# Kernel optimization log

Measured on AMD Instinct MI355X. Metric: run time of the kernel, lower is better.

The kernel has to match this reference:

```python
import jax, jax.numpy as jnp
import numpy as np

E, H, L = 512, 1024, 2
SRC_V, TGT_V = 32000, 32000
B, S, T = 32, 128, 128
BOS = 1  # vocab.Vocab.bos_idx


def _lstm_layer(x, h0, c0, Wih, Whh, bih, bhh):
    """Single-direction LSTM layer. x: [B, S, D] -> (ys [B,S,H], hT, cT).
    PyTorch gate order: i, f, g, o."""
    b = bih + bhh
    def step(carry, xt):
        h, c = carry
        gates = xt @ Wih.T + h @ Whh.T + b          # [B, 4H]
        i, f, g, o = jnp.split(gates, 4, axis=-1)
        i = jax.nn.sigmoid(i)
        f = jax.nn.sigmoid(f)
        g = jnp.tanh(g)
        o = jax.nn.sigmoid(o)
        c = f * c + i * g
        h = o * jnp.tanh(c)
        return (h, c), h
    (hT, cT), ys = jax.lax.scan(step, (h0, c0), jnp.swapaxes(x, 0, 1))
    return jnp.swapaxes(ys, 0, 1), hT, cT


def _stacked_lstm(x, h0s, c0s, params):
    """params: list of (Wih, Whh, bih, bhh) per layer. h0s/c0s: [L, B, H]."""
    hs, cs = [], []
    y = x
    for l, (Wih, Whh, bih, bhh) in enumerate(params):
        y, hT, cT = _lstm_layer(y, h0s[l], c0s[l], Wih, Whh, bih, bhh)
        hs.append(hT)
        cs.append(cT)
    return y, jnp.stack(hs), jnp.stack(cs)


def setup_inputs() -> dict:
    key = jax.random.key(0)
    ks = jax.random.split(key, 24)
    sc = 1.0 / np.sqrt(H)
    inp = {}
    inp["src"] = jax.random.randint(ks[0], (B, S), 0, SRC_V)
    inp["tgt"] = jax.random.randint(ks[1], (B, T), 0, TGT_V)
    inp["enc_emb"] = jax.random.normal(ks[2], (SRC_V, E), jnp.float32)
    inp["dec_emb"] = jax.random.normal(ks[3], (TGT_V, E), jnp.float32)
    i = 4
    for pre in ("enc", "dec"):
        for l in range(L):
            din = E if l == 0 else H
            inp[f"{pre}_Wih{l}"] = jax.random.uniform(ks[i + 0], (4 * H, din), jnp.float32, -sc, sc)
            inp[f"{pre}_Whh{l}"] = jax.random.uniform(ks[i + 1], (4 * H, H), jnp.float32, -sc, sc)
            inp[f"{pre}_bih{l}"] = jax.random.uniform(ks[i + 2], (4 * H,), jnp.float32, -sc, sc)
            inp[f"{pre}_bhh{l}"] = jax.random.uniform(ks[i + 3], (4 * H,), jnp.float32, -sc, sc)
            i += 4
    return inp


def reference(src, tgt, enc_emb, dec_emb,
              enc_Wih0, enc_Whh0, enc_bih0, enc_bhh0,
              enc_Wih1, enc_Whh1, enc_bih1, enc_bhh1,
              dec_Wih0, dec_Whh0, dec_bih0, dec_bhh0,
              dec_Wih1, dec_Whh1, dec_bih1, dec_bhh1):
    enc_params = [(enc_Wih0, enc_Whh0, enc_bih0, enc_bhh0),
                  (enc_Wih1, enc_Whh1, enc_bih1, enc_bhh1)]
    dec_params = [(dec_Wih0, dec_Whh0, dec_bih0, dec_bhh0),
                  (dec_Wih1, dec_Whh1, dec_bih1, dec_bhh1)]
    # Encoder: full-sequence LSTM from zero state
    x = enc_emb[src]                                  # [B, S, E]
    zeros = jnp.zeros((L, B, H), x.dtype)
    enc_out, h, c = _stacked_lstm(x, zeros, zeros, enc_params)
    # Decoder: teacher-forced inputs = [BOS, tgt[:, :-1]]
    dec_in = jnp.concatenate(
        [jnp.full((B, 1), BOS, tgt.dtype), tgt[:, :-1]], axis=1)  # [B, T]
    y = dec_emb[dec_in]                               # [B, T, E]
    dec_out, _, _ = _stacked_lstm(y, h, c, dec_params)
    return dec_out                                    # [B, T, H]
```

## Files before the change

### kernel.cpp

```cpp
#include <hip/hip_runtime.h>
#include <hip/hip_bf16.h>
#include <stdint.h>


typedef __attribute__((ext_vector_type(8))) __bf16 bf16x8;
typedef __attribute__((ext_vector_type(4))) __bf16 bf16x4;
typedef __attribute__((ext_vector_type(4))) float  f32x4;

#define SLAB 32768
#define RNN_SMEM (65536 + 65536 + 512)

__device__ __forceinline__ float sigmoidf_(float x) {
  return 1.f / (1.f + __expf(-x));
}
__device__ __forceinline__ float tanhf_(float x) {
  float e = __expf(-2.f * fabsf(x));
  float t = (1.f - e) / (1.f + e);
  return x < 0.f ? -t : t;
}

__global__ void init_ws(float* zeros, unsigned* flags) {
  int i = blockIdx.x * 256 + threadIdx.x;
  if (i < 32 * 1024) zeros[i] = 0.f;
  if (i < 512) flags[i] = 0u;
}

__global__ void gather_emb(const int* __restrict__ src, const int* __restrict__ tgt,
                           const float* __restrict__ ee, const float* __restrict__ de,
                           __bf16* __restrict__ Xe, __bf16* __restrict__ Xd) {
  int row = blockIdx.x & 4095;
  int t = row >> 5, b = row & 31;
  bool isd = blockIdx.x >= 4096;
  int tok = isd ? (t == 0 ? 1 : tgt[b * 128 + t - 1]) : src[b * 128 + t];
  const float* ep = (isd ? de : ee) + (size_t)tok * 512;
  __bf16* op = (isd ? Xd : Xe) + (size_t)row * 512;
  int i = threadIdx.x * 4;
  float4 v = *(const float4*)(ep + i);
  bf16x4 t4;
  t4[0] = (__bf16)v.x; t4[1] = (__bf16)v.y; t4[2] = (__bf16)v.z; t4[3] = (__bf16)v.w;
  *(bf16x4*)(op + i) = t4;
}

__global__ __launch_bounds__(256) void gemm_xp(
    const __bf16* __restrict__ A, const float* __restrict__ W,
    const float* __restrict__ bih, const float* __restrict__ bhh,
    __bf16* __restrict__ C, int K) {
  __shared__ char sA[128 * 64 * 2];
  __shared__ char sB[128 * 64 * 2];
  int tid = threadIdx.x;
  int lane = tid & 63, wave = tid >> 6;
  int wm = wave & 1, wn = wave >> 1;
  int bm = blockIdx.x & 31, bn = blockIdx.x >> 5;
  int frow = lane & 15;
  int kj = (lane >> 4) * 16;

  f32x4 acc[4][4] = {};

  for (int k0 = 0; k0 < K; k0 += 64) {
#pragma unroll
    for (int c4 = 0; c4 < 4; ++c4) {
      int idx = (c4 * 256 + tid) * 8;
      int r = idx >> 6, kk = idx & 63;
      bf16x8 v = *(const bf16x8*)(A + (size_t)(bm * 128 + r) * K + k0 + kk);
      *(bf16x8*)(sA + ((r * 128 + kk * 2) ^ ((r & 7) << 4))) = v;
    }
#pragma unroll
    for (int c4 = 0; c4 < 4; ++c4) {
      int idx = (c4 * 256 + tid) * 8;
      int r = idx >> 6, kk = idx & 63;
      const float* wp = W + (size_t)(bn * 128 + r) * K + k0 + kk;
      float4 w0 = *(const float4*)wp;
      float4 w1 = *(const float4*)(wp + 4);
      bf16x8 v;
      v[0] = (__bf16)w0.x; v[1] = (__bf16)w0.y; v[2] = (__bf16)w0.z; v[3] = (__bf16)w0.w;
      v[4] = (__bf16)w1.x; v[5] = (__bf16)w1.y; v[6] = (__bf16)w1.z; v[7] = (__bf16)w1.w;
      *(bf16x8*)(sB + ((r * 128 + kk * 2) ^ ((r & 7) << 4))) = v;
    }
    __syncthreads();
#pragma unroll
    for (int half = 0; half < 2; ++half) {
      int kb = half * 64 + kj;
      bf16x8 af[4], bfr[4];
#pragma unroll
      for (int f = 0; f < 4; ++f) {
        int arr = wm * 64 + f * 16 + frow;
        af[f] = *(const bf16x8*)(sA + (arr * 128 + (kb ^ ((arr & 7) << 4))));
        int brr = wn * 64 + f * 16 + frow;
        bfr[f] = *(const bf16x8*)(sB + (brr * 128 + (kb ^ ((brr & 7) << 4))));
      }
#pragma unroll
      for (int fm = 0; fm < 4; ++fm)
#pragma unroll
        for (int fn = 0; fn < 4; ++fn)
          acc[fm][fn] = __builtin_amdgcn_mfma_f32_16x16x32_bf16(af[fm], bfr[fn],
                                                                acc[fm][fn], 0, 0, 0);
    }
    __syncthreads();
  }
  int cm = bm * 128 + wm * 64, cn = bn * 128 + wn * 64;
#pragma unroll
  for (int fn = 0; fn < 4; ++fn) {
    int col = cn + fn * 16 + frow;
    int g = col >> 10, hcol = col & 1023;
    int blkd = hcol >> 3, hl = hcol & 7;
    float bias = bih[col] + bhh[col];
#pragma unroll
    for (int fm = 0; fm < 4; ++fm) {
      int r0 = cm + fm * 16 + ((lane >> 4) << 2);
#pragma unroll
      for (int j = 0; j < 4; ++j) {
        int row = r0 + j;
        C[(size_t)(row >> 5) * 131072 + blkd * 1024 + hl * 128 + g * 32 +
          (row & 31)] = (__bf16)(acc[fm][fn][j] + bias);
      }
    }
  }
}

struct RnnArgs {
  const float* Whh;
  const float* Wxh;
  const float* bih;
  const float* bhh;
  const __bf16* XP;
  const __bf16* xslab;
  const unsigned* xflags;
  const __bf16* h0;
  const float* c0;
  __bf16* hseq;
  float* cfin;
  float* yout;
  unsigned* flags;
};

__device__ __forceinline__ void wait128(const unsigned* fl, unsigned t) {
  int lane = threadIdx.x & 63;
  for (;;) {
    bool ok = (__hip_atomic_load(fl + lane, __ATOMIC_RELAXED,
                                 __HIP_MEMORY_SCOPE_AGENT) >= t) &&
              (__hip_atomic_load(fl + 64 + lane, __ATOMIC_RELAXED,
                                 __HIP_MEMORY_SCOPE_AGENT) >= t);
    if (__all(ok)) return;
    __builtin_amdgcn_s_sleep(1);
  }
}

__device__ __forceinline__ f32x4 accum_k1024_sw(f32x4 acc, const char* bbase,
                                                const char* aRow, int swz, int kj) {
#pragma unroll
  for (int kt = 0; kt < 32; kt += 8) {
    bf16x8 bv[8];
#pragma unroll
    for (int u = 0; u < 8; ++u)
      bv[u] = *(const bf16x8*)(bbase + (size_t)(kt + u) * 2048);
#pragma unroll
    for (int u = 0; u < 8; ++u) {
      int kb = (kt + u) * 64 + kj;
      bf16x8 av = *(const bf16x8*)(aRow + (kb ^ swz));
      acc = __builtin_amdgcn_mfma_f32_16x16x32_bf16(av, bv[u], acc, 0, 0, 0);
    }
  }
  return acc;
}

__device__ __forceinline__ void rnn_body(const RnnArgs& P, int blk, char* smem) {
  char*   sW0 = smem;
  char*   sW1 = smem + 65536;
  __bf16* sP  = (__bf16*)(smem + 131072);

  int tid = threadIdx.x;
  int lane = tid & 63, wave = tid >> 6;
  int mt = wave & 1, nt = wave >> 1;
  bool isL0 = (P.XP != nullptr);

  __builtin_amdgcn_fence(__ATOMIC_ACQUIRE, "agent");

  {
    const float* srcs[2] = {P.Wxh, P.Whh};
    char* dsts[2] = {sW0, sW1};
    for (int s = (isL0 ? 1 : 0); s < 2; ++s) {
      for (int g = 0; g < 4; ++g) {
        const float* sp = srcs[s] + (size_t)(g * 1024 + blk * 8) * 1024;
#pragma unroll
        for (int it = 0; it < 8; ++it) {
          int e = (it * 256 + tid) * 4;
          int rl = e >> 10, k = e & 1023;
          float4 v = *(const float4*)(sp + e);
          bf16x4 t4;
          t4[0] = (__bf16)v.x; t4[1] = (__bf16)v.y;
          t4[2] = (__bf16)v.z; t4[3] = (__bf16)v.w;
          int r = rl * 4 + g;
          *(bf16x4*)(dsts[s] + ((r << 11) + ((k << 1) ^ ((r & 7) << 4)))) = t4;
        }
      }
    }
  }

  int hl = mt * 4 + (lane >> 4);
  int b  = nt * 16 + (lane & 15);
  float c = P.c0[b * 1024 + blk * 8 + hl];

  float bI = 0.f, bF = 0.f, bG = 0.f, bO = 0.f;
  if (!isL0) {
    int col = blk * 8 + hl;
    bI = P.bih[col] + P.bhh[col];
    bF = P.bih[1024 + col] + P.bhh[1024 + col];
    bG = P.bih[2048 + col] + P.bhh[2048 + col];
    bO = P.bih[3072 + col] + P.bhh[3072 + col];
  }

  int rr  = mt * 16 + (lane & 15);
  int swz = (rr & 7) << 4;
  const char* aRow0 = sW0 + (rr << 11);
  const char* aRow1 = sW1 + (rr << 11);
  int kj   = (lane >> 4) * 16;
  int bsub = (lane >> 4) * 512 + b * 16;

  const __bf16* xpb = isL0 ? (P.XP + (size_t)blk * 1024 + hl * 128 + b) : nullptr;

  for (int t = 0; t < 128; ++t) {
    float xi = bI, xf = bF, xg = bG, xo = bO;
    if (isL0) {
      const __bf16* xr = xpb + (size_t)t * 131072;
      xi = (float)xr[0];  xf = (float)xr[32];
      xg = (float)xr[64]; xo = (float)xr[96];
    }

    const char* hb = (const char*)((t == 0) ? P.h0
                                            : (P.hseq + (size_t)(t - 1) * SLAB)) + bsub;
    f32x4 acc = {0.f, 0.f, 0.f, 0.f};

    if (isL0) {
      if (wave == 0 && t > 0) wait128(P.flags, (unsigned)t);
      __syncthreads();
      acc = accum_k1024_sw(acc, hb, aRow1, swz, kj);
    } else {
      if (wave == 0) wait128(P.xflags, (unsigned)(t + 1));
      __syncthreads();
      const char* xb = (const char*)(P.xslab + (size_t)t * SLAB) + bsub;
      acc = accum_k1024_sw(acc, xb, aRow0, swz, kj);
      if (wave == 0 && t > 0) wait128(P.flags, (unsigned)t);
      __syncthreads();
      acc = accum_k1024_sw(acc, hb, aRow1, swz, kj);
    }

    float gi = sigmoidf_(acc[0] + xi);
    float gf = sigmoidf_(acc[1] + xf);
    float gg = tanhf_(acc[2] + xg);
    float go = sigmoidf_(acc[3] + xo);
    c = gf * c + gi * gg;
    float h = go * tanhf_(c);
    sP[b * 8 + hl] = (__bf16)h;
    __syncthreads();

    if (tid < 64) {
      unsigned long long v = *(const unsigned long long*)(sP + tid * 4);
      unsigned long long* dst = (unsigned long long*)(
          (char*)P.hseq + (size_t)t * 65536 + blk * 512 + tid * 8);
      __hip_atomic_store(dst, v, __ATOMIC_RELAXED, __HIP_MEMORY_SCOPE_AGENT);
      asm volatile("s_waitcnt vmcnt(0)" ::: "memory");
      if (tid == 0)
        __hip_atomic_store(P.flags + blk, (unsigned)(t + 1), __ATOMIC_RELEASE,
                           __HIP_MEMORY_SCOPE_AGENT);
    }
    if (P.yout) {
      int yb = tid >> 3, yhl = tid & 7;
      P.yout[((size_t)yb * 128 + t) * 1024 + blk * 8 + yhl] =
          (float)sP[yb * 8 + yhl];
    }
  }
  P.cfin[b * 1024 + blk * 8 + hl] = c;
}

__global__ __launch_bounds__(256) void rnn_pair(RnnArgs A, RnnArgs B) {
  extern __shared__ char smem[];
  if (blockIdx.x < 128) rnn_body(A, blockIdx.x, smem);
  else                  rnn_body(B, blockIdx.x - 128, smem);
}

extern "C" void kernel_launch(void* const* d_in, const int* in_sizes, int n_in,
                              void* d_out, int out_size, void* d_ws, size_t ws_size,
                              hipStream_t stream) {
  (void)in_sizes; (void)n_in; (void)out_size; (void)ws_size;
  const int*   src     = (const int*)d_in[0];
  const int*   tgt     = (const int*)d_in[1];
  const float* enc_emb = (const float*)d_in[2];
  const float* dec_emb = (const float*)d_in[3];
  const float* W[16];
  for (int i = 0; i < 16; ++i) W[i] = (const float*)d_in[4 + i];

  char* ws = (char*)d_ws;
  size_t off = 0;
  auto alloc = [&](size_t bytes) {
    char* p = ws + off;
    off += (bytes + 255) & ~(size_t)255;
    return p;
  };
  unsigned* flags = (unsigned*)alloc((size_t)4 * 128 * sizeof(unsigned));
  float*    zeros = (float*)alloc((size_t)32 * 1024 * 4);
  __bf16*   Xe   = (__bf16*)alloc((size_t)4096 * 512 * 2);
  __bf16*   Xd   = (__bf16*)alloc((size_t)4096 * 512 * 2);
  __bf16*   XP1  = (__bf16*)alloc((size_t)4096 * 4096 * 2);
  __bf16*   XP2  = (__bf16*)alloc((size_t)4096 * 4096 * 2);
  __bf16*   hE0  = (__bf16*)alloc((size_t)128 * SLAB * 2);
  __bf16*   hE1  = (__bf16*)alloc((size_t)128 * SLAB * 2);
  __bf16*   hD0  = (__bf16*)alloc((size_t)128 * SLAB * 2);
  __bf16*   hD1  = (__bf16*)alloc((size_t)128 * SLAB * 2);
  float*    cE0  = (float*)alloc((size_t)32 * 1024 * 4);
  float*    cE1  = (float*)alloc((size_t)32 * 1024 * 4);
  float*    cd0  = (float*)alloc((size_t)32 * 1024 * 4);
  float*    cd1  = (float*)alloc((size_t)32 * 1024 * 4);

  hipFuncSetAttribute((const void*)rnn_pair,
                      hipFuncAttributeMaxDynamicSharedMemorySize, RNN_SMEM);

  init_ws<<<128, 256, 0, stream>>>(zeros, flags);
  gather_emb<<<8192, 128, 0, stream>>>(src, tgt, enc_emb, dec_emb, Xe, Xd);

  gemm_xp<<<1024, 256, 0, stream>>>(Xe, W[0], W[2], W[3], XP1, 512);
  gemm_xp<<<1024, 256, 0, stream>>>(Xd, W[8], W[10], W[11], XP2, 512);

  unsigned* fE0 = flags;
  unsigned* fE1 = flags + 128;
  unsigned* fD0 = flags + 256;
  unsigned* fD1 = flags + 384;

  RnnArgs e0{W[1], nullptr, nullptr, nullptr, XP1, nullptr, nullptr,
             (const __bf16*)zeros, zeros, hE0, cE0, nullptr, fE0};
  RnnArgs e1{W[5], W[4], W[6], W[7], nullptr, hE0, fE0,
             (const __bf16*)zeros, zeros, hE1, cE1, nullptr, fE1};
  rnn_pair<<<256, 256, RNN_SMEM, stream>>>(e0, e1);

  RnnArgs d0{W[9], nullptr, nullptr, nullptr, XP2, nullptr, nullptr,
             hE0 + (size_t)127 * SLAB, cE0, hD0, cd0, nullptr, fD0};
  RnnArgs d1{W[13], W[12], W[14], W[15], nullptr, hD0, fD0,
             hE1 + (size_t)127 * SLAB, cE1, hD1, cd1, (float*)d_out, fD1};
  rnn_pair<<<256, 256, RNN_SMEM, stream>>>(d0, d1);
}
```

Before: 2.141 ms.

## Prefetch layer-1 input slab into registers one step ahead and merge waits

Splits the recurrent body into separate layer-0 and layer-1 paths. The layer-1 path double-buffers its input-slab fragments in registers, loading step t+1's x data after finishing step t. It also merges the xflags and flags spin-waits into a single poll and drops one barrier per step. Launch bounds are set to one block per SM so the larger register footprint (64 bf16x8 fragments plus h fragments) fits, at the risk of register pressure or spills.

```diff
diff --git a/kernel.cpp b/kernel.cpp
--- a/kernel.cpp
+++ b/kernel.cpp
@@ -216,63 +216,139 @@
   int kj   = (lane >> 4) * 16;
   int bsub = (lane >> 4) * 512 + b * 16;
 
-  const __bf16* xpb = isL0 ? (P.XP + (size_t)blk * 1024 + hl * 128 + b) : nullptr;
-
-  for (int t = 0; t < 128; ++t) {
-    float xi = bI, xf = bF, xg = bG, xo = bO;
-    if (isL0) {
+  if (isL0) {
+    const __bf16* xpb = P.XP + (size_t)blk * 1024 + hl * 128 + b;
+    for (int t = 0; t < 128; ++t) {
       const __bf16* xr = xpb + (size_t)t * 131072;
-      xi = (float)xr[0];  xf = (float)xr[32];
-      xg = (float)xr[64]; xo = (float)xr[96];
-    }
-
-    const char* hb = (const char*)((t == 0) ? P.h0
-                                            : (P.hseq + (size_t)(t - 1) * SLAB)) + bsub;
-    f32x4 acc = {0.f, 0.f, 0.f, 0.f};
-
-    if (isL0) {
+      float pxi = (float)xr[0];  float pxf = (float)xr[32];
+      float pxg = (float)xr[64]; float pxo = (float)xr[96];
+
+      const char* hb = (const char*)((t == 0) ? P.h0
+                         : (P.hseq + (size_t)(t - 1) * SLAB)) + bsub;
+      f32x4 acc = {0.f, 0.f, 0.f, 0.f};
+
       if (wave == 0 && t > 0) wait128(P.flags, (unsigned)t);
       __syncthreads();
       acc = accum_k1024_sw(acc, hb, aRow1, swz, kj);
-    } else {
-      if (wave == 0) wait128(P.xflags, (unsigned)(t + 1));
+
+      float gi = sigmoidf_(acc[0] + pxi);
+      float gf = sigmoidf_(acc[1] + pxf);
+      float gg = tanhf_(acc[2] + pxg);
+      float go = sigmoidf_(acc[3] + pxo);
+      c = gf * c + gi * gg;
+      float h = go * tanhf_(c);
+      sP[b * 8 + hl] = (__bf16)h;
       __syncthreads();
-      const char* xb = (const char*)(P.xslab + (size_t)t * SLAB) + bsub;
-      acc = accum_k1024_sw(acc, xb, aRow0, swz, kj);
-      if (wave == 0 && t > 0) wait128(P.flags, (unsigned)t);
-      __syncthreads();
-      acc = accum_k1024_sw(acc, hb, aRow1, swz, kj);
-    }
-
-    float gi = sigmoidf_(acc[0] + xi);
-    float gf = sigmoidf_(acc[1] + xf);
-    float gg = tanhf_(acc[2] + xg);
-    float go = sigmoidf_(acc[3] + xo);
-    c = gf * c + gi * gg;
-    float h = go * tanhf_(c);
-    sP[b * 8 + hl] = (__bf16)h;
+
+      if (tid < 64) {
+        unsigned long long v = *(const unsigned long long*)(sP + tid * 4);
+        unsigned long long* dst = (unsigned long long*)(
+            (char*)P.hseq + (size_t)t * 65536 + blk * 512 + tid * 8);
+        __hip_atomic_store(dst, v, __ATOMIC_RELAXED, __HIP_MEMORY_SCOPE_AGENT);
+        asm volatile("s_waitcnt vmcnt(0)" ::: "memory");
+        if (tid == 0)
+          __hip_atomic_store(P.flags + blk, (unsigned)(t + 1), __ATOMIC_RELEASE,
+                             __HIP_MEMORY_SCOPE_AGENT);
+      }
+    }
+  } else {
+    bf16x8 xfA[32], xfB[32];
+
+    if (wave == 0) wait128(P.xflags, 1u);
     __syncthreads();
-
-    if (tid < 64) {
-      unsigned long long v = *(const unsigned long long*)(sP + tid * 4);
-      unsigned long long* dst = (unsigned long long*)(
-          (char*)P.hseq + (size_t)t * 65536 + blk * 512 + tid * 8);
-      __hip_atomic_store(dst, v, __ATOMIC_RELAXED, __HIP_MEMORY_SCOPE_AGENT);
-      asm volatile("s_waitcnt vmcnt(0)" ::: "memory");
-      if (tid == 0)
-        __hip_atomic_store(P.flags + blk, (unsigned)(t + 1), __ATOMIC_RELEASE,
-                           __HIP_MEMORY_SCOPE_AGENT);
-    }
-    if (P.yout) {
-      int yb = tid >> 3, yhl = tid & 7;
-      P.yout[((size_t)yb * 128 + t) * 1024 + blk * 8 + yhl] =
-          (float)sP[yb * 8 + yhl];
-    }
-  }
+    {
+      const char* xb = (const char*)P.xslab + bsub;
+#pragma unroll
+      for (int u = 0; u < 32; ++u)
+        xfA[u] = *(const bf16x8*)(xb + (size_t)u * 2048);
+    }
+
+#define L1_STEP(T, XC, XN)                                                    \
+  {                                                                           \
+    const int t = (T);                                                        \
+            \
+    if (wave == 0) {                                                          \
+      unsigned th = (unsigned)t;                                              \
+      unsigned tx = (unsigned)(t + 2 < 128 ? t + 2 : 128);                    \
+      for (;;) {                                                              \
+        bool ok = (__hip_atomic_load(P.xflags + lane, __ATOMIC_RELAXED,       \
+                                     __HIP_MEMORY_SCOPE_AGENT) >= tx) &&      \
+                  (__hip_atomic_load(P.xflags + 64 + lane, __ATOMIC_RELAXED,  \
+                                     __HIP_MEMORY_SCOPE_AGENT) >= tx);        \
+        if (t > 0)                                                            \
+          ok = ok &&                                                          \
+               (__hip_atomic_load(P.flags + lane, __ATOMIC_RELAXED,           \
+                                  __HIP_MEMORY_SCOPE_AGENT) >= th) &&         \
+               (__hip_atomic_load(P.flags + 64 + lane, __ATOMIC_RELAXED,      \
+                                  __HIP_MEMORY_SCOPE_AGENT) >= th);           \
+        if (__all(ok)) break;                                                 \
+        __builtin_amdgcn_s_sleep(1);                                          \
+      }                                                                       \
+    }                                                                         \
+    __syncthreads();                                                          \
+                                 \
+    const char* hb = (const char*)((t == 0) ? P.h0                            \
+                       : (P.hseq + (size_t)(t - 1) * SLAB)) + bsub;           \
+    bf16x8 hf[32];                                                            \
+    _Pragma("unroll") for (int u = 0; u < 32; ++u)                            \
+        hf[u] = *(const bf16x8*)(hb + (size_t)u * 2048);                      \
+                         \
+    f32x4 acc = {0.f, 0.f, 0.f, 0.f};                                         \
+    _Pragma("unroll") for (int u = 0; u < 32; ++u) {                          \
+      int kb = u * 64 + kj;                                                   \
+      bf16x8 av = *(const bf16x8*)(aRow0 + (kb ^ swz));                       \
+      acc = __builtin_amdgcn_mfma_f32_16x16x32_bf16(av, XC[u], acc, 0, 0, 0); \
+    }                                                                         \
+                                     \
+    _Pragma("unroll") for (int u = 0; u < 32; ++u) {                          \
+      int kb = u * 64 + kj;                                                   \
+      bf16x8 av = *(const bf16x8*)(aRow1 + (kb ^ swz));                       \
+      acc = __builtin_amdgcn_mfma_f32_16x16x32_bf16(av, hf[u], acc, 0, 0, 0); \
+    }                                                                         \
+                          \
+    float gi = sigmoidf_(acc[0] + bI);                                        \
+    float gf = sigmoidf_(acc[1] + bF);                                        \
+    float gg = tanhf_(acc[2] + bG);                                           \
+    float go = sigmoidf_(acc[3] + bO);                                        \
+    c = gf * c + gi * gg;                                                     \
+    float h = go * tanhf_(c);                                                 \
+    sP[b * 8 + hl] = (__bf16)h;                                               \
+    __syncthreads();                                                          \
+    if (tid < 64) {                                                           \
+      unsigned long long v = *(const unsigned long long*)(sP + tid * 4);      \
+      unsigned long long* dst = (unsigned long long*)(                        \
+          (char*)P.hseq + (size_t)t * 65536 + blk * 512 + tid * 8);           \
+      __hip_atomic_store(dst, v, __ATOMIC_RELAXED, __HIP_MEMORY_SCOPE_AGENT); \
+      asm volatile("s_waitcnt vmcnt(0)" ::: "memory");                        \
+      if (tid == 0)                                                           \
+        __hip_atomic_store(P.flags + blk, (unsigned)(t + 1),                  \
+                           __ATOMIC_RELEASE, __HIP_MEMORY_SCOPE_AGENT);       \
+    }                                                                         \
+    if (P.yout) {                                                             \
+      int yb = tid >> 3, yhl = tid & 7;                                       \
+      P.yout[((size_t)yb * 128 + t) * 1024 + blk * 8 + yhl] =                 \
+          (float)sP[yb * 8 + yhl];                                            \
+    }                                                                         \
+        \
+    {                                                                         \
+      int pidx = (t + 1 < 128) ? (t + 1) : 127;                               \
+      const char* xnb = (const char*)(P.xslab + (size_t)pidx * SLAB) + bsub;  \
+      _Pragma("unroll") for (int u = 0; u < 32; ++u)                          \
+          XN[u] = *(const bf16x8*)(xnb + (size_t)u * 2048);                   \
+    }                                                                         \
+  }
+
+    for (int t2 = 0; t2 < 128; t2 += 2) {
+      L1_STEP(t2, xfA, xfB)
+      L1_STEP(t2 + 1, xfB, xfA)
+    }
+#undef L1_STEP
+  }
+
   P.cfin[b * 1024 + blk * 8 + hl] = c;
 }
 
-__global__ __launch_bounds__(256) void rnn_pair(RnnArgs A, RnnArgs B) {
+__global__ __launch_bounds__(256, 1) void rnn_pair(RnnArgs A, RnnArgs B) {
   extern __shared__ char smem[];
   if (blockIdx.x < 128) rnn_body(A, blockIdx.x, smem);
   else                  rnn_body(B, blockIdx.x - 128, smem);
```

Result: slower. 2.366 ms (+10.5%).
